# Performance work log

Hardware: AMD Instinct MI355X
Metric: run time of the kernel (lower is better)

Reference implementation:

```python
import jax, jax.numpy as jnp
import numpy as np

EPS_AGG = 1e-6  # torch code adds 1e-6 to scatter weight sums
EPS_BN = 1e-5


def _pix_idx(loc_orig, H, W):
    # map normalized coords in [-1,1] to flat pixel index on an HxW grid
    loc = jnp.clip(loc_orig, -1.0, 1.0) * 0.5 + 0.5
    ix = jnp.round(loc[..., 0] * (W - 1)).astype(jnp.int32)
    iy = jnp.round(loc[..., 1] * (H - 1)).astype(jnp.int32)
    return iy * W + ix  # [B, N0]


def token2map(x, loc_orig, idx_agg, H, W):
    # scatter token features to a dense map, averaging collisions
    B, N, C = x.shape
    N0 = idx_agg.shape[1]
    idx_hw = _pix_idx(loc_orig, H, W)                                   # [B, N0]
    tok = jnp.take_along_axis(x, idx_agg[..., None], axis=1)            # [B, N0, C]
    flat = (idx_hw + jnp.arange(B, dtype=jnp.int32)[:, None] * (H * W)).reshape(-1)
    sums = jax.ops.segment_sum(tok.reshape(-1, C), flat, num_segments=B * H * W)
    cnt = jax.ops.segment_sum(jnp.ones((B * N0,), x.dtype), flat, num_segments=B * H * W)
    out = sums / (cnt[:, None] + EPS_AGG)
    return out.reshape(B, H, W, C).transpose(0, 3, 1, 2)                # [B, C, H, W]


def map2token(fmap, Nt, loc_orig, idx_agg_t, agg_weight_t):
    # gather map pixels back to Nt target tokens, weighted-averaging per token
    B, C, H, W = fmap.shape
    idx_hw = _pix_idx(loc_orig, H, W)                                   # [B, N0]
    pix = fmap.transpose(0, 2, 3, 1).reshape(B, H * W, C)
    gath = jnp.take_along_axis(pix, idx_hw[..., None], axis=1)          # [B, N0, C]
    flat = (idx_agg_t + jnp.arange(B, dtype=jnp.int32)[:, None] * Nt).reshape(-1)
    num = jax.ops.segment_sum((gath * agg_weight_t[..., None]).reshape(-1, C), flat, num_segments=B * Nt)
    den = jax.ops.segment_sum(agg_weight_t.reshape(-1), flat, num_segments=B * Nt)
    return (num / (den[:, None] + EPS_AGG)).reshape(B, Nt, C)


def token_downup(x, idx_agg_s, idx_agg_t, agg_weight_t, Nt):
    # weighted aggregation from N source tokens to Nt target tokens via N0 original positions
    B, N, C = x.shape
    src = jnp.take_along_axis(x, idx_agg_s[..., None], axis=1)          # [B, N0, C]
    flat = (idx_agg_t + jnp.arange(B, dtype=jnp.int32)[:, None] * Nt).reshape(-1)
    num = jax.ops.segment_sum((src * agg_weight_t[..., None]).reshape(-1, C), flat, num_segments=B * Nt)
    den = jax.ops.segment_sum(agg_weight_t.reshape(-1), flat, num_segments=B * Nt)
    return (num / (den[:, None] + EPS_AGG)).reshape(B, Nt, C)


def batchnorm(x, gamma, beta):
    # BatchNorm2d on [B,C,Nt,1] == per-channel stats over (B, Nt); x here is [B, Nt, C]
    mu = x.mean(axis=(0, 1), keepdims=True)
    var = x.var(axis=(0, 1), keepdims=True)
    return (x - mu) * jax.lax.rsqrt(var + EPS_BN) * gamma + beta


def setup_inputs() -> dict:
    key = jax.random.key(0)
    ks = jax.random.split(key, 12)
    B, N, N0, Nt, Cin, Cout, H, W = 32, 1568, 3136, 784, 256, 512, 56, 56
    x = jax.random.normal(ks[0], (B, N, Cin), dtype=jnp.float32)
    loc_orig = jax.random.uniform(ks[1], (B, N0, 2), dtype=jnp.float32, minval=-1.0, maxval=1.0)
    idx_agg = jax.random.randint(ks[2], (B, N0), 0, N, dtype=jnp.int32)
    agg_weight = jax.random.uniform(ks[3], (B, N0), dtype=jnp.float32)
    idx_agg_t = jax.random.randint(ks[4], (B, N0), 0, Nt, dtype=jnp.int32)
    agg_weight_t = jax.random.uniform(ks[5], (B, N0), dtype=jnp.float32)
    dw_w = jax.random.normal(ks[6], (Cin, 1, 3, 3), dtype=jnp.float32) * 0.1     # depthwise 3x3
    skip_w = jax.random.normal(ks[7], (Cin,), dtype=jnp.float32) * 0.1           # depthwise 1x1
    conv_w = jax.random.normal(ks[8], (Cout, Cin), dtype=jnp.float32) * (1.0 / np.sqrt(Cin))
    gamma1 = jnp.ones((Cin,), jnp.float32); beta1 = jnp.zeros((Cin,), jnp.float32)
    gamma2 = jnp.ones((Cout,), jnp.float32); beta2 = jnp.zeros((Cout,), jnp.float32)
    return {"x": x, "loc_orig": loc_orig, "idx_agg": idx_agg, "agg_weight": agg_weight,
            "idx_agg_t": idx_agg_t, "agg_weight_t": agg_weight_t, "H": H, "W": W, "Nt": Nt,
            "dw_w": dw_w, "skip_w": skip_w, "conv_w": conv_w,
            "gamma1": gamma1, "beta1": beta1, "gamma2": gamma2, "beta2": beta2}


def reference(x, loc_orig, idx_agg, agg_weight, idx_agg_t, agg_weight_t, H, W, Nt,
              dw_w, skip_w, conv_w, gamma1, beta1, gamma2, beta2):
    # token -> map scatter
    x_map = token2map(x, loc_orig, idx_agg, H, W)                       # [B, Cin, H, W]
    # 3x3 depthwise conv, stride 2, padding 1
    Cin = x_map.shape[1]
    x_map = jax.lax.conv_general_dilated(
        x_map, dw_w, window_strides=(2, 2), padding=((1, 1), (1, 1)),
        feature_group_count=Cin, dimension_numbers=("NCHW", "OIHW", "NCHW"))    # [B, Cin, H/2, W/2]
    # map -> target tokens gather
    x_back = map2token(x_map, Nt, loc_orig, idx_agg_t, agg_weight_t)    # [B, Nt, Cin]
    # skip path: token downsample + 1x1 depthwise (per-channel scale)
    xs = token_downup(x, idx_agg, idx_agg_t, agg_weight_t, Nt)          # [B, Nt, Cin]
    xs = xs * skip_w                                                    # dw_skip, groups=Cin, k=1
    y = xs + x_back
    y = batchnorm(y, gamma1, beta1)
    y = jnp.einsum("bnc,oc->bno", y, conv_w)                            # 1x1 conv Cin->Cout
    y = batchnorm(y, gamma2, beta2)
    return jax.nn.relu(y)                                               # [B, Nt, Cout]
```

## Files before the change

### kernel.cpp

```cpp
#include <hip/hip_runtime.h>

constexpr int B    = 32;
constexpr int N    = 1568;
constexpr int N0   = 3136;
constexpr int Nt   = 784;
constexpr int Cin  = 256;
constexpr int Cout = 512;
constexpr int H    = 56;
constexpr int W    = 56;
constexpr int HW   = 3136;
constexpr int Ho   = 28;
constexpr int Wo   = 28;
constexpr int HWo  = 784;
constexpr int RR   = B * Nt;
constexpr int NE   = B * N0;
constexpr int NBP  = B * HW;
constexpr int NBT  = B * Nt;
constexpr int NBO  = B * HWo;
constexpr int SB   = NBT + NBO;
constexpr int NCHUNK = SB / 256;
constexpr int NG   = 32;

constexpr size_t W_HISTP = 0;
constexpr size_t W_HISTS = NBP;
constexpr size_t W_S2SUM = NBP + SB;
constexpr size_t W_S2SQ  = W_S2SUM + Cout;
constexpr size_t W_S1P   = W_S2SQ + Cout;
constexpr size_t W_S1QP  = W_S1P + (size_t)NG * Cin;
constexpr size_t W_MEND  = W_S1QP + (size_t)NG * Cin;
constexpr size_t W_OFF   = W_MEND;
constexpr size_t W_CUR   = W_OFF + SB + 8;
constexpr size_t W_PC    = W_CUR + SB;
constexpr size_t W_BSUM  = W_PC + NE;
constexpr size_t W_LT    = W_BSUM + 512;
constexpr size_t W_LC    = W_LT + (size_t)2 * NE;
constexpr size_t W_CONVB = W_LC + (size_t)8 * NE;
constexpr size_t W_YBF   = W_CONVB + (size_t)B * HWo * Cin / 2;
constexpr size_t W_WFB   = W_YBF + (size_t)RR * Cin / 2;
constexpr size_t W_BIAS  = W_WFB + (size_t)Cout * Cin / 2;
constexpr size_t W_ZB    = W_BIAS + Cout;

__device__ __forceinline__ int pix_of(float t, float scale) {
    t = fminf(fmaxf(t, -1.0f), 1.0f);
    float u = __fadd_rn(__fmul_rn(t, 0.5f), 0.5f);
    return (int)rintf(__fmul_rn(u, scale));
}
__device__ __forceinline__ unsigned short f2bf(float f) {
    unsigned int u = __float_as_uint(f);
    u = (u + 0x7fffu + ((u >> 16) & 1u)) >> 16;
    return (unsigned short)u;
}
__device__ __forceinline__ float bf2f(unsigned short h) {
    return __uint_as_float(((unsigned int)h) << 16);
}
__device__ __forceinline__ void gload_lds16(const void* g, void* lds) {
    __builtin_amdgcn_global_load_lds(
        (const __attribute__((address_space(1))) void*)g,
        (__attribute__((address_space(3))) void*)lds, 16, 0, 0);
}

__global__ void k_hist(const float* __restrict__ loc, const int* __restrict__ idxt,
                       int* __restrict__ histP, int* __restrict__ histS,
                       int* __restrict__ pc) {
    int i = blockIdx.x * 256 + threadIdx.x;
    if (i >= NE) return;
    int b = i / N0;
    float lx = loc[(size_t)2 * i], ly = loc[(size_t)2 * i + 1];
    int ix = pix_of(lx, 55.0f), iy = pix_of(ly, 55.0f);
    int jx = pix_of(lx, 27.0f), jy = pix_of(ly, 27.0f);
    int p56 = iy * W + ix, p28 = jy * Wo + jx;
    pc[i] = p56 | (p28 << 16);
    atomicAdd(&histP[b * HW + p56], 1);
    atomicAdd(&histS[b * Nt + idxt[i]], 1);
    int oy_lo = iy >> 1, oy_hi = min(Ho - 1, (iy + 1) >> 1);
    int ox_lo = ix >> 1, ox_hi = min(Wo - 1, (ix + 1) >> 1);
    for (int oy = oy_lo; oy <= oy_hi; ++oy)
        for (int ox = ox_lo; ox <= ox_hi; ++ox)
            atomicAdd(&histS[NBT + b * HWo + oy * Wo + ox], 1);
}

__global__ void k_scanA(const int* __restrict__ hist, int* __restrict__ bsum) {
    __shared__ int sm[256];
    int i = blockIdx.x * 256 + threadIdx.x;
    sm[threadIdx.x] = hist[i];
    __syncthreads();
    for (int d = 128; d > 0; d >>= 1) {
        if (threadIdx.x < d) sm[threadIdx.x] += sm[threadIdx.x + d];
        __syncthreads();
    }
    if (threadIdx.x == 0) bsum[blockIdx.x] = sm[0];
}

__global__ void k_scanB(int* __restrict__ bsum) {
    __shared__ int sm[512];
    int t = threadIdx.x;
    int v = (t < NCHUNK) ? bsum[t] : 0;
    sm[t] = v; __syncthreads();
    for (int d = 1; d < 512; d <<= 1) {
        int u = (t >= d) ? sm[t - d] : 0;
        __syncthreads();
        sm[t] += u;
        __syncthreads();
    }
    if (t < NCHUNK) bsum[t] = sm[t] - v;
}

__global__ void k_scanC(const int* __restrict__ hist, const int* __restrict__ bsum,
                        int* __restrict__ off, int* __restrict__ cur) {
    __shared__ int sm[256];
    int t = threadIdx.x;
    int i = blockIdx.x * 256 + t;
    int v = hist[i];
    sm[t] = v; __syncthreads();
    for (int d = 1; d < 256; d <<= 1) {
        int u = (t >= d) ? sm[t - d] : 0;
        __syncthreads();
        sm[t] += u;
        __syncthreads();
    }
    int excl = bsum[blockIdx.x] + sm[t] - v;
    off[i] = excl; cur[i] = excl;
    if (i == SB - 1) off[SB] = excl + v;
}

__global__ void k_scat(const int* __restrict__ pc, const int* __restrict__ idxa,
                       const int* __restrict__ idxt, const float* __restrict__ wt,
                       const int* __restrict__ histP, int* __restrict__ cur,
                       int2* __restrict__ listT, int2* __restrict__ listC) {
    int i = blockIdx.x * 256 + threadIdx.x;
    if (i >= NE) return;
    int b = i / N0;
    int v = pc[i];
    int p56 = v & 0xFFFF, p28 = v >> 16;
    int s = idxa[i];
    int posT = atomicAdd(&cur[b * Nt + idxt[i]], 1);
    listT[posT] = make_int2(s | (p28 << 16), __float_as_int(wt[i]));
    float wrc = 1.0f / ((float)histP[b * HW + p56] + 1e-6f);
    int wrci = __float_as_int(wrc);
    int iy = p56 / W, ix = p56 - iy * W;
    int oy_lo = iy >> 1, oy_hi = min(Ho - 1, (iy + 1) >> 1);
    int ox_lo = ix >> 1, ox_hi = min(Wo - 1, (ix + 1) >> 1);
    for (int oy = oy_lo; oy <= oy_hi; ++oy)
        for (int ox = ox_lo; ox <= ox_hi; ++ox) {
            int tap = (iy - (2 * oy - 1)) * 3 + (ix - (2 * ox - 1));
            int posC = atomicAdd(&cur[NBT + b * HWo + oy * Wo + ox], 1) - NE;
            listC[posC] = make_int2(s | (tap << 16), wrci);
        }
}

__global__ __launch_bounds__(256) void k_gconv(const float* __restrict__ x,
        const int* __restrict__ off, const int2* __restrict__ listC,
        const float* __restrict__ dww, unsigned short* __restrict__ convb) {
    __shared__ float wsm[9 * 256];
    int t = threadIdx.x;
#pragma unroll
    for (int k = 0; k < 9; ++k) wsm[k * 256 + t] = dww[t * 9 + k];
    int wv = t >> 6, lane = t & 63;
    int blk = blockIdx.x * 4 + wv;
    int b   = __builtin_amdgcn_readfirstlane(blk / HWo);
    int st  = __builtin_amdgcn_readfirstlane(off[NBT + blk]) - NE;
    int en  = __builtin_amdgcn_readfirstlane(off[NBT + blk + 1]) - NE;
    __syncthreads();
    const float* xb = x + (size_t)b * N * Cin;
    float4 acc = make_float4(0.f, 0.f, 0.f, 0.f);
    for (int base = st; base < en; base += 64) {
        int n = en - base; if (n > 64) n = 64;
        int2 e = make_int2(0, 0);
        if (lane < n) e = listC[base + lane];
        int j = 0;
        for (; j + 4 <= n; j += 4) {
            int ex0 = __builtin_amdgcn_readlane(e.x, j + 0);
            int ey0 = __builtin_amdgcn_readlane(e.y, j + 0);
            int ex1 = __builtin_amdgcn_readlane(e.x, j + 1);
            int ey1 = __builtin_amdgcn_readlane(e.y, j + 1);
            int ex2 = __builtin_amdgcn_readlane(e.x, j + 2);
            int ey2 = __builtin_amdgcn_readlane(e.y, j + 2);
            int ex3 = __builtin_amdgcn_readlane(e.x, j + 3);
            int ey3 = __builtin_amdgcn_readlane(e.y, j + 3);
            float4 v0 = ((const float4*)(xb + (size_t)(ex0 & 0xFFFF) * Cin))[lane];
            float4 v1 = ((const float4*)(xb + (size_t)(ex1 & 0xFFFF) * Cin))[lane];
            float4 v2 = ((const float4*)(xb + (size_t)(ex2 & 0xFFFF) * Cin))[lane];
            float4 v3 = ((const float4*)(xb + (size_t)(ex3 & 0xFFFF) * Cin))[lane];
            float4 w0 = *(const float4*)&wsm[(ex0 >> 16) * 256 + lane * 4];
            float4 w1 = *(const float4*)&wsm[(ex1 >> 16) * 256 + lane * 4];
            float4 w2 = *(const float4*)&wsm[(ex2 >> 16) * 256 + lane * 4];
            float4 w3 = *(const float4*)&wsm[(ex3 >> 16) * 256 + lane * 4];
            float r0 = __int_as_float(ey0), r1 = __int_as_float(ey1);
            float r2 = __int_as_float(ey2), r3 = __int_as_float(ey3);
            acc.x = fmaf(v0.x * r0, w0.x, acc.x);
            acc.y = fmaf(v0.y * r0, w0.y, acc.y);
            acc.z = fmaf(v0.z * r0, w0.z, acc.z);
            acc.w = fmaf(v0.w * r0, w0.w, acc.w);
            acc.x = fmaf(v1.x * r1, w1.x, acc.x);
            acc.y = fmaf(v1.y * r1, w1.y, acc.y);
            acc.z = fmaf(v1.z * r1, w1.z, acc.z);
            acc.w = fmaf(v1.w * r1, w1.w, acc.w);
            acc.x = fmaf(v2.x * r2, w2.x, acc.x);
            acc.y = fmaf(v2.y * r2, w2.y, acc.y);
            acc.z = fmaf(v2.z * r2, w2.z, acc.z);
            acc.w = fmaf(v2.w * r2, w2.w, acc.w);
            acc.x = fmaf(v3.x * r3, w3.x, acc.x);
            acc.y = fmaf(v3.y * r3, w3.y, acc.y);
            acc.z = fmaf(v3.z * r3, w3.z, acc.z);
            acc.w = fmaf(v3.w * r3, w3.w, acc.w);
        }
        for (; j < n; ++j) {
            int ex = __builtin_amdgcn_readlane(e.x, j);
            int ey = __builtin_amdgcn_readlane(e.y, j);
            float4 v = ((const float4*)(xb + (size_t)(ex & 0xFFFF) * Cin))[lane];
            float4 wq = *(const float4*)&wsm[(ex >> 16) * 256 + lane * 4];
            float r = __int_as_float(ey);
            acc.x = fmaf(v.x * r, wq.x, acc.x);
            acc.y = fmaf(v.y * r, wq.y, acc.y);
            acc.z = fmaf(v.z * r, wq.z, acc.z);
            acc.w = fmaf(v.w * r, wq.w, acc.w);
        }
    }
    uint2 o;
    o.x = (unsigned int)f2bf(acc.x) | ((unsigned int)f2bf(acc.y) << 16);
    o.y = (unsigned int)f2bf(acc.z) | ((unsigned int)f2bf(acc.w) << 16);
    ((uint2*)(convb + (size_t)blk * Cin))[lane] = o;
}

__global__ __launch_bounds__(256) void k_gtok(const float* __restrict__ x,
        const unsigned short* __restrict__ convb, const int* __restrict__ off,
        const int2* __restrict__ listT, const float* __restrict__ skipw,
        unsigned short* __restrict__ ybf, float* __restrict__ s1p,
        float* __restrict__ s1qp) {
    __shared__ float smS[4][256];
    __shared__ float smQ[4][256];
    int t = threadIdx.x, wv = t >> 6, lane = t & 63;
    int bt = blockIdx.x * 4 + wv;
    int b  = __builtin_amdgcn_readfirstlane(bt / Nt);
    int st = __builtin_amdgcn_readfirstlane(off[bt]);
    int en = __builtin_amdgcn_readfirstlane(off[bt + 1]);
    const float* xb = x + (size_t)b * N * Cin;
    const unsigned short* cbb = convb + (size_t)b * HWo * Cin;
    float4 sk = ((const float4*)skipw)[lane];
    float4 acc = make_float4(0.f, 0.f, 0.f, 0.f);
    float wsum = 0.0f;
    for (int base = st; base < en; base += 64) {
        int n = en - base; if (n > 64) n = 64;
        int2 e = make_int2(0, 0);
        if (lane < n) e = listT[base + lane];
        int j = 0;
        for (; j + 2 <= n; j += 2) {
            int ex0 = __builtin_amdgcn_readlane(e.x, j + 0);
            int ey0 = __builtin_amdgcn_readlane(e.y, j + 0);
            int ex1 = __builtin_amdgcn_readlane(e.x, j + 1);
            int ey1 = __builtin_amdgcn_readlane(e.y, j + 1);
            float4 xv0 = ((const float4*)(xb + (size_t)(ex0 & 0xFFFF) * Cin))[lane];
            float4 xv1 = ((const float4*)(xb + (size_t)(ex1 & 0xFFFF) * Cin))[lane];
            uint2 cv0 = ((const uint2*)(cbb + (size_t)(ex0 >> 16) * Cin))[lane];
            uint2 cv1 = ((const uint2*)(cbb + (size_t)(ex1 >> 16) * Cin))[lane];
            float w0 = __int_as_float(ey0), w1 = __int_as_float(ey1);
            wsum += w0 + w1;
            acc.x = fmaf(w0, bf2f((unsigned short)(cv0.x & 0xffffu)) + sk.x * xv0.x, acc.x);
            acc.y = fmaf(w0, bf2f((unsigned short)(cv0.x >> 16))     + sk.y * xv0.y, acc.y);
            acc.z = fmaf(w0, bf2f((unsigned short)(cv0.y & 0xffffu)) + sk.z * xv0.z, acc.z);
            acc.w = fmaf(w0, bf2f((unsigned short)(cv0.y >> 16))     + sk.w * xv0.w, acc.w);
            acc.x = fmaf(w1, bf2f((unsigned short)(cv1.x & 0xffffu)) + sk.x * xv1.x, acc.x);
            acc.y = fmaf(w1, bf2f((unsigned short)(cv1.x >> 16))     + sk.y * xv1.y, acc.y);
            acc.z = fmaf(w1, bf2f((unsigned short)(cv1.y & 0xffffu)) + sk.z * xv1.z, acc.z);
            acc.w = fmaf(w1, bf2f((unsigned short)(cv1.y >> 16))     + sk.w * xv1.w, acc.w);
        }
        for (; j < n; ++j) {
            int ex = __builtin_amdgcn_readlane(e.x, j);
            int ey = __builtin_amdgcn_readlane(e.y, j);
            float4 xv = ((const float4*)(xb + (size_t)(ex & 0xFFFF) * Cin))[lane];
            uint2 cv = ((const uint2*)(cbb + (size_t)(ex >> 16) * Cin))[lane];
            float w = __int_as_float(ey);
            wsum += w;
            acc.x = fmaf(w, bf2f((unsigned short)(cv.x & 0xffffu)) + sk.x * xv.x, acc.x);
            acc.y = fmaf(w, bf2f((unsigned short)(cv.x >> 16))     + sk.y * xv.y, acc.y);
            acc.z = fmaf(w, bf2f((unsigned short)(cv.y & 0xffffu)) + sk.z * xv.z, acc.z);
            acc.w = fmaf(w, bf2f((unsigned short)(cv.y >> 16))     + sk.w * xv.w, acc.w);
        }
    }
    float rw = 1.0f / (wsum + 1e-6f);
    float y0 = acc.x * rw, y1 = acc.y * rw, y2 = acc.z * rw, y3 = acc.w * rw;
    smS[wv][lane * 4 + 0] = y0; smQ[wv][lane * 4 + 0] = y0 * y0;
    smS[wv][lane * 4 + 1] = y1; smQ[wv][lane * 4 + 1] = y1 * y1;
    smS[wv][lane * 4 + 2] = y2; smQ[wv][lane * 4 + 2] = y2 * y2;
    smS[wv][lane * 4 + 3] = y3; smQ[wv][lane * 4 + 3] = y3 * y3;
    uint2 o;
    o.x = (unsigned int)f2bf(y0) | ((unsigned int)f2bf(y1) << 16);
    o.y = (unsigned int)f2bf(y2) | ((unsigned int)f2bf(y3) << 16);
    ((uint2*)(ybf + (size_t)bt * Cin))[lane] = o;
    __syncthreads();
    float ps = smS[0][t] + smS[1][t] + smS[2][t] + smS[3][t];
    float pq = smQ[0][t] + smQ[1][t] + smQ[2][t] + smQ[3][t];
    int g = (blockIdx.x & (NG - 1)) * Cin + t;
    atomicAdd(&s1p[g],  ps);
    atomicAdd(&s1qp[g], pq);
}

__global__ void k_fold(const float* __restrict__ s1p, const float* __restrict__ s1qp,
                       const float* __restrict__ g1, const float* __restrict__ b1,
                       const float* __restrict__ convw, unsigned short* __restrict__ wfb,
                       float* __restrict__ bias) {
    int o = blockIdx.x, c = threadIdx.x;
    const float inv = 1.0f / (float)RR;
    float s = 0.0f, q = 0.0f;
#pragma unroll
    for (int g = 0; g < NG; ++g) { s += s1p[g * Cin + c]; q += s1qp[g * Cin + c]; }
    float mu  = s * inv;
    float var = q * inv - mu * mu;
    float a   = g1[c] / sqrtf(var + 1e-5f);
    float bs  = b1[c] - mu * a;
    float wv  = convw[(size_t)o * Cin + c];
    wfb[(size_t)o * Cin + c] = f2bf(wv * a);
    __shared__ float red[256];
    red[c] = wv * bs;
    __syncthreads();
    for (int st = 128; st > 0; st >>= 1) {
        if (c < st) red[c] += red[c + st];
        __syncthreads();
    }
    if (c == 0) bias[o] = red[0];
}

typedef __attribute__((ext_vector_type(8))) short short8;
typedef __attribute__((ext_vector_type(4))) float f32x4;

__global__ __launch_bounds__(256, 1) void k_gemm(const unsigned short* __restrict__ A,
        const unsigned short* __restrict__ Bt, const float* __restrict__ bias,
        unsigned short* __restrict__ zb, float* __restrict__ s2, float* __restrict__ s2q) {
    __shared__ unsigned short As[128 * 256];
    __shared__ unsigned short Bs[128 * 256];
    __shared__ float rsum[128], rsq[128];
    int m0 = blockIdx.x * 128, n0 = blockIdx.y * 128;
    int t = threadIdx.x;
    int wave = t >> 6, lane = t & 63;
    int wm = wave >> 1, wn = wave & 1;
    int l16 = lane & 15, lq = lane >> 4;
    if (t < 128) { rsum[t] = 0.0f; rsq[t] = 0.0f; }

    {
        int rlo = lane >> 5;
        int ch  = lane & 31;
#pragma unroll
        for (int p = 0; p < 16; ++p) {
            int row = wave * 32 + p * 2 + rlo;
            int sc  = ch ^ (row & 7);
            gload_lds16(A + (size_t)(m0 + row) * Cin + sc * 8,
                        &As[(wave * 32 + p * 2) * 256]);
        }
#pragma unroll
        for (int p = 0; p < 16; ++p) {
            int row = wave * 32 + p * 2 + rlo;
            int sc  = ch ^ (row & 7);
            gload_lds16(Bt + (size_t)(n0 + row) * Cin + sc * 8,
                        &Bs[(wave * 32 + p * 2) * 256]);
        }
    }
    asm volatile("s_waitcnt vmcnt(0)" ::: "memory");
    __syncthreads();

    f32x4 acc[4][4];
#pragma unroll
    for (int i = 0; i < 4; ++i)
#pragma unroll
        for (int j = 0; j < 4; ++j) acc[i][j] = (f32x4)0.0f;

#pragma unroll
    for (int ks = 0; ks < 8; ++ks) {
        short8 af[4], bf[4];
#pragma unroll
        for (int i = 0; i < 4; ++i) {
            int row = wm * 64 + i * 16 + l16;
            int c   = (ks * 4 + lq) ^ (row & 7);
            af[i] = *(short8*)&As[row * 256 + c * 8];
        }
#pragma unroll
        for (int j = 0; j < 4; ++j) {
            int row = wn * 64 + j * 16 + l16;
            int c   = (ks * 4 + lq) ^ (row & 7);
            bf[j] = *(short8*)&Bs[row * 256 + c * 8];
        }
#pragma unroll
        for (int i = 0; i < 4; ++i)
#pragma unroll
            for (int j = 0; j < 4; ++j)
                acc[i][j] = __builtin_amdgcn_mfma_f32_16x16x32_bf16(af[i], bf[j], acc[i][j], 0, 0, 0);
    }

#pragma unroll
    for (int j = 0; j < 4; ++j) {
        int cl  = wn * 64 + j * 16 + l16;
        int col = n0 + cl;
        float bv = bias[col];
        float ps = 0.0f, pq = 0.0f;
#pragma unroll
        for (int i = 0; i < 4; ++i) {
            int rbase = m0 + wm * 64 + i * 16 + lq * 4;
#pragma unroll
            for (int r = 0; r < 4; ++r) {
                float v = acc[i][j][r] + bv;
                zb[(size_t)(rbase + r) * Cout + col] = f2bf(v);
                ps += v;
                pq = fmaf(v, v, pq);
            }
        }
        atomicAdd(&rsum[cl], ps);
        atomicAdd(&rsq[cl], pq);
    }
    __syncthreads();
    if (t < 128) {
        atomicAdd(&s2[n0 + t], rsum[t]);
        atomicAdd(&s2q[n0 + t], rsq[t]);
    }
}

__global__ void k_final(const unsigned short* __restrict__ zb,
                        const float* __restrict__ s2, const float* __restrict__ s2q,
                        const float* __restrict__ g2, const float* __restrict__ b2,
                        float* __restrict__ out) {
    size_t j4 = ((size_t)blockIdx.x * 256 + threadIdx.x) * 4;
    int o = (int)(j4 & (Cout - 1));
    const float inv = 1.0f / (float)RR;
    uint2 u = *(const uint2*)&zb[j4];
    float e0 = bf2f((unsigned short)(u.x & 0xffffu));
    float e1 = bf2f((unsigned short)(u.x >> 16));
    float e2 = bf2f((unsigned short)(u.y & 0xffffu));
    float e3 = bf2f((unsigned short)(u.y >> 16));
    float mu0 = s2[o + 0] * inv, a0 = g2[o + 0] * rsqrtf(s2q[o + 0] * inv - mu0 * mu0 + 1e-5f);
    float mu1 = s2[o + 1] * inv, a1 = g2[o + 1] * rsqrtf(s2q[o + 1] * inv - mu1 * mu1 + 1e-5f);
    float mu2 = s2[o + 2] * inv, a2 = g2[o + 2] * rsqrtf(s2q[o + 2] * inv - mu2 * mu2 + 1e-5f);
    float mu3 = s2[o + 3] * inv, a3 = g2[o + 3] * rsqrtf(s2q[o + 3] * inv - mu3 * mu3 + 1e-5f);
    float c0 = b2[o + 0] - mu0 * a0;
    float c1 = b2[o + 1] - mu1 * a1;
    float c2 = b2[o + 2] - mu2 * a2;
    float c3 = b2[o + 3] - mu3 * a3;
    float4 r;
    r.x = fmaxf(fmaf(e0, a0, c0), 0.0f);
    r.y = fmaxf(fmaf(e1, a1, c1), 0.0f);
    r.z = fmaxf(fmaf(e2, a2, c2), 0.0f);
    r.w = fmaxf(fmaf(e3, a3, c3), 0.0f);
    *(float4*)&out[j4] = r;
}

extern "C" void kernel_launch(void* const* d_in, const int* in_sizes, int n_in,
                              void* d_out, int out_size, void* d_ws, size_t ws_size,
                              hipStream_t stream) {
    const float* x     = (const float*)d_in[0];
    const float* loc   = (const float*)d_in[1];
    const int*   idxa  = (const int*)d_in[2];
    const int*   idxt  = (const int*)d_in[4];
    const float* wt    = (const float*)d_in[5];
    const float* dww   = (const float*)d_in[9];
    const float* skipw = (const float*)d_in[10];
    const float* convw = (const float*)d_in[11];
    const float* g1    = (const float*)d_in[12];
    const float* b1    = (const float*)d_in[13];
    const float* g2    = (const float*)d_in[14];
    const float* b2    = (const float*)d_in[15];

    float* ws = (float*)d_ws;
    int*   histP = (int*)(ws + W_HISTP);
    int*   histS = (int*)(ws + W_HISTS);
    float* s2sum = ws + W_S2SUM;
    float* s2sq  = ws + W_S2SQ;
    float* s1p   = ws + W_S1P;
    float* s1qp  = ws + W_S1QP;
    int*   off   = (int*)(ws + W_OFF);
    int*   cur   = (int*)(ws + W_CUR);
    int*   pc    = (int*)(ws + W_PC);
    int*   bsum  = (int*)(ws + W_BSUM);
    int2*  listT = (int2*)(ws + W_LT);
    int2*  listC = (int2*)(ws + W_LC);
    unsigned short* convb = (unsigned short*)(ws + W_CONVB);
    unsigned short* ybf   = (unsigned short*)(ws + W_YBF);
    unsigned short* wfb   = (unsigned short*)(ws + W_WFB);
    float* bias  = ws + W_BIAS;
    unsigned short* zb = (unsigned short*)(ws + W_ZB);
    float* out   = (float*)d_out;

    hipMemsetAsync(histP, 0, (size_t)W_MEND * sizeof(float), stream);

    k_hist<<<NE / 256, 256, 0, stream>>>(loc, idxt, histP, histS, pc);
    k_scanA<<<NCHUNK, 256, 0, stream>>>(histS, bsum);
    k_scanB<<<1, 512, 0, stream>>>(bsum);
    k_scanC<<<NCHUNK, 256, 0, stream>>>(histS, bsum, off, cur);
    k_scat<<<NE / 256, 256, 0, stream>>>(pc, idxa, idxt, wt, histP, cur, listT, listC);

    k_gconv<<<NBO / 4, 256, 0, stream>>>(x, off, listC, dww, convb);
    k_gtok<<<NBT / 4, 256, 0, stream>>>(x, convb, off, listT, skipw, ybf, s1p, s1qp);
    k_fold<<<Cout, 256, 0, stream>>>(s1p, s1qp, g1, b1, convw, wfb, bias);

    dim3 gg(RR / 128, Cout / 128);
    k_gemm<<<gg, 256, 0, stream>>>(ybf, wfb, bias, zb, s2sum, s2sq);
    k_final<<<(int)(((size_t)RR * Cout) / 1024), 256, 0, stream>>>(zb, s2sum, s2sq, g2, b2, out);
}
```

Baseline: 255.8 us.

## Double-buffer GEMM K-tiles in LDS and raise occupancy

The bf16 MFMA GEMM no longer stages the full K=256 slices of A and B into LDS up front. It now streams 32-wide K tiles through two small LDS buffers, prefetching the next tile while MFMAs run on the current one, with a new XOR swizzle matched to the narrower rows. The LDS footprint drops from about 128KB to about 16KB, and launch bounds are raised to allow 4 blocks per CU. The aim is to hide global-load latency and let more blocks share a CU, at the cost of a barrier per K step. The GEMM is only one part of the whole pipeline, so its effect on total time is limited.

```diff
diff --git a/kernel.cpp b/kernel.cpp
--- a/kernel.cpp
+++ b/kernel.cpp
@@ -323,11 +323,11 @@
 typedef __attribute__((ext_vector_type(8))) short short8;
 typedef __attribute__((ext_vector_type(4))) float f32x4;
 
-__global__ __launch_bounds__(256, 1) void k_gemm(const unsigned short* __restrict__ A,
+__global__ __launch_bounds__(256, 4) void k_gemm(const unsigned short* __restrict__ A,
         const unsigned short* __restrict__ Bt, const float* __restrict__ bias,
         unsigned short* __restrict__ zb, float* __restrict__ s2, float* __restrict__ s2q) {
-    __shared__ unsigned short As[128 * 256];
-    __shared__ unsigned short Bs[128 * 256];
+    __shared__ unsigned short As[2][128 * 32];
+    __shared__ unsigned short Bs[2][128 * 32];
     __shared__ float rsum[128], rsq[128];
     int m0 = blockIdx.x * 128, n0 = blockIdx.y * 128;
     int t = threadIdx.x;
@@ -336,26 +336,22 @@
     int l16 = lane & 15, lq = lane >> 4;
     if (t < 128) { rsum[t] = 0.0f; rsq[t] = 0.0f; }
 
-    {
-        int rlo = lane >> 5;
-        int ch  = lane & 31;
-#pragma unroll
-        for (int p = 0; p < 16; ++p) {
-            int row = wave * 32 + p * 2 + rlo;
-            int sc  = ch ^ (row & 7);
-            gload_lds16(A + (size_t)(m0 + row) * Cin + sc * 8,
-                        &As[(wave * 32 + p * 2) * 256]);
-        }
-#pragma unroll
-        for (int p = 0; p < 16; ++p) {
-            int row = wave * 32 + p * 2 + rlo;
-            int sc  = ch ^ (row & 7);
-            gload_lds16(Bt + (size_t)(n0 + row) * Cin + sc * 8,
-                        &Bs[(wave * 32 + p * 2) * 256]);
-        }
-    }
-    asm volatile("s_waitcnt vmcnt(0)" ::: "memory");
-    __syncthreads();
+    int r_off = lane >> 2;
+    int sc    = (lane & 3) ^ ((lane >> 4) & 3);
+    const unsigned short* Asrc = A  + (size_t)(m0 + r_off) * Cin + sc * 8;
+    const unsigned short* Bsrc = Bt + (size_t)(n0 + r_off) * Cin + sc * 8;
+    int r0a = wave * 32, r0b = r0a + 16;
+
+    auto STAGE = [&](int buf, int k0) {
+        gload_lds16(Asrc + (size_t)r0a * Cin + k0, &As[buf][r0a * 32]);
+        gload_lds16(Asrc + (size_t)r0b * Cin + k0, &As[buf][r0b * 32]);
+        gload_lds16(Bsrc + (size_t)r0a * Cin + k0, &Bs[buf][r0a * 32]);
+        gload_lds16(Bsrc + (size_t)r0b * Cin + k0, &Bs[buf][r0b * 32]);
+    };
+
+    int ckoff = (lq ^ ((l16 >> 2) & 3)) * 8;
+    int rbA = (wm * 64 + l16) * 32 + ckoff;
+    int rbB = (wn * 64 + l16) * 32 + ckoff;
 
     f32x4 acc[4][4];
 #pragma unroll
@@ -363,26 +359,23 @@
 #pragma unroll
         for (int j = 0; j < 4; ++j) acc[i][j] = (f32x4)0.0f;
 
+    STAGE(0, 0);
+    __syncthreads();
 #pragma unroll
     for (int ks = 0; ks < 8; ++ks) {
+        int cur = ks & 1;
+        if (ks < 7) STAGE(cur ^ 1, (ks + 1) * 32);
         short8 af[4], bf[4];
 #pragma unroll
-        for (int i = 0; i < 4; ++i) {
-            int row = wm * 64 + i * 16 + l16;
-            int c   = (ks * 4 + lq) ^ (row & 7);
-            af[i] = *(short8*)&As[row * 256 + c * 8];
-        }
-#pragma unroll
-        for (int j = 0; j < 4; ++j) {
-            int row = wn * 64 + j * 16 + l16;
-            int c   = (ks * 4 + lq) ^ (row & 7);
-            bf[j] = *(short8*)&Bs[row * 256 + c * 8];
-        }
+        for (int i = 0; i < 4; ++i) af[i] = *(short8*)&As[cur][rbA + i * 512];
+#pragma unroll
+        for (int j = 0; j < 4; ++j) bf[j] = *(short8*)&Bs[cur][rbB + j * 512];
 #pragma unroll
         for (int i = 0; i < 4; ++i)
 #pragma unroll
             for (int j = 0; j < 4; ++j)
                 acc[i][j] = __builtin_amdgcn_mfma_f32_16x16x32_bf16(af[i], bf[j], acc[i][j], 0, 0, 0);
+        __syncthreads();
     }
 
 #pragma unroll
```

After: 248.0 us. 1.03x faster.
